# Kernel tuning notes

Hardware: AMD Instinct MI355X
Metric: run time of the kernel (lower is better)

The kernel has to match this reference:

```python
import jax, jax.numpy as jnp
import numpy as np

N_EMBED = 1024
N_HEAD = 16
HEAD_SIZE = N_EMBED // N_HEAD  # 64
SEQ = 2048
BATCH = 2
EPS = 1e-5


def setup_inputs() -> dict:
    key = jax.random.key(0)
    ks = jax.random.split(key, 16)
    s = lambda fan_in: 1.0 / np.sqrt(fan_in)
    d, h, hs, f = N_EMBED, N_HEAD, HEAD_SIZE, 4 * N_EMBED
    return {
        "x": jax.random.normal(ks[0], (BATCH, SEQ, d), dtype=jnp.float32),
        # per-head QKV projections (no bias), stacked over heads: [H, D, hs]
        "wq": jax.random.normal(ks[1], (h, d, hs), dtype=jnp.float32) * s(d),
        "wk": jax.random.normal(ks[2], (h, d, hs), dtype=jnp.float32) * s(d),
        "wv": jax.random.normal(ks[3], (h, d, hs), dtype=jnp.float32) * s(d),
        "w_proj": jax.random.normal(ks[4], (d, d), dtype=jnp.float32) * s(d),
        "b_proj": jnp.zeros((d,), dtype=jnp.float32),
        "w1": jax.random.normal(ks[5], (d, f), dtype=jnp.float32) * s(d),
        "b1": jnp.zeros((f,), dtype=jnp.float32),
        "w2": jax.random.normal(ks[6], (f, d), dtype=jnp.float32) * s(f),
        "b2": jnp.zeros((d,), dtype=jnp.float32),
        "g1": jnp.ones((d,), dtype=jnp.float32),
        "be1": jnp.zeros((d,), dtype=jnp.float32),
        "g2": jnp.ones((d,), dtype=jnp.float32),
        "be2": jnp.zeros((d,), dtype=jnp.float32),
    }


def _layer_norm(x, gamma, beta):
    mu = jnp.mean(x, axis=-1, keepdims=True)
    var = jnp.mean(jnp.square(x - mu), axis=-1, keepdims=True)
    return (x - mu) * jax.lax.rsqrt(var + EPS) * gamma + beta


def reference(x, wq, wk, wv, w_proj, b_proj, w1, b1, w2, b2, g1, be1, g2, be2):
    B, S, D = x.shape
    # per-head projections (vectorized over heads): [B, H, S, hs]
    q = jnp.einsum("bsd,hdk->bhsk", x, wq)
    k = jnp.einsum("bsd,hdk->bhsk", x, wk)
    v = jnp.einsum("bsd,hdk->bhsk", x, wv)
    scale = HEAD_SIZE ** -0.5
    scores = jnp.einsum("bhsk,bhtk->bhst", q, k) * scale  # [B,H,S,S]
    causal = jnp.tril(jnp.ones((S, S), dtype=bool))
    scores = jnp.where(causal, scores, -jnp.inf)
    w = jax.nn.softmax(scores, axis=-1)  # dropout=0 -> identity
    attn = jnp.einsum("bhst,bhtk->bhsk", w, v)  # [B,H,S,hs]
    # concat heads (head-major ordering matches torch.cat over heads)
    attn = attn.transpose(0, 2, 1, 3).reshape(B, S, D)
    y = attn @ w_proj + b_proj
    x = _layer_norm(x + y, g1, be1)
    y = jax.nn.relu(x @ w1 + b1) @ w2 + b2
    x = _layer_norm(x + y, g2, be2)
    return x
```

## Files before the change

kernel.cpp:

```cpp
#include <hip/hip_runtime.h>


typedef unsigned short u16;
typedef unsigned int u32;
typedef __attribute__((ext_vector_type(8))) short bf16x8;
typedef __attribute__((ext_vector_type(4))) float f32x4;
typedef __attribute__((ext_vector_type(2))) u32 u32x2;
typedef __attribute__((ext_vector_type(4))) _Float16 f16x4;

#define MFMA16(a, b, c) __builtin_amdgcn_mfma_f32_16x16x32_bf16(a, b, c, 0, 0, 0)
#define MFMAH(a, b, c) __builtin_amdgcn_mfma_f32_16x16x16f16(a, b, c, 0, 0, 0)

__device__ __forceinline__ u16 f2b(float f) {
  unsigned int u = __builtin_bit_cast(unsigned int, f);
  u = (u + 0x7fffu + ((u >> 16) & 1u)) >> 16;
  return (u16)u;
}

__device__ __forceinline__ void gload_lds16(const u16* g, u16* l) {
  __builtin_amdgcn_global_load_lds((const __attribute__((address_space(1))) void*)g,
                                   (__attribute__((address_space(3))) void*)l, 16, 0, 0);
}

__device__ __forceinline__ u32 pkrtz(float lo, float hi) {
  return __builtin_bit_cast(u32, __builtin_amdgcn_cvt_pkrtz(lo, hi));
}

__device__ __forceinline__ f16x4 pack4h(float a, float b, float c, float d) {
  u32x2 r = {pkrtz(a, b), pkrtz(c, d)};
  return __builtin_bit_cast(f16x4, r);
}


__global__ __launch_bounds__(256) void castx_kernel(const float* __restrict__ src,
                                                    u16* __restrict__ dst) {
  int i = (blockIdx.x * 256 + threadIdx.x) * 4;
  float4 v = *(const float4*)(src + i);
  dst[i + 0] = f2b(v.x);
  dst[i + 1] = f2b(v.y);
  dst[i + 2] = f2b(v.z);
  dst[i + 3] = f2b(v.w);
}

__global__ __launch_bounds__(256) void tcast_kernel(const float* __restrict__ src,
                                                    u16* __restrict__ dst, int R, int C) {
  __shared__ float tile[32][33];
  int tx = threadIdx.x, ty = threadIdx.y;
  int r0 = blockIdx.y * 32, c0 = blockIdx.x * 32;
#pragma unroll
  for (int i = 0; i < 4; ++i)
    tile[ty + i * 8][tx] = src[(size_t)(r0 + ty + i * 8) * C + c0 + tx];
  __syncthreads();
#pragma unroll
  for (int i = 0; i < 4; ++i)
    dst[(size_t)(c0 + ty + i * 8) * R + r0 + tx] = f2b(tile[tx][ty + i * 8]);
}

__global__ __launch_bounds__(256) void tcast_qkv_kernel(const float* __restrict__ wq,
                                                        const float* __restrict__ wk,
                                                        const float* __restrict__ wv,
                                                        u16* __restrict__ dst) {
  __shared__ float tile[32][33];
  int tx = threadIdx.x, ty = threadIdx.y;
  int z = blockIdx.z;
  int p = z >> 4, h = z & 15;
  const float* src = (p == 0 ? wq : (p == 1 ? wk : wv)) + (size_t)h * 1024 * 64;
  float scale = (p == 0) ? 0.1803368801f : 1.0f;
  u16* dbase = dst + (size_t)(p * 1024 + h * 64) * 1024;
  int r0 = blockIdx.y * 32, c0 = blockIdx.x * 32;
#pragma unroll
  for (int i = 0; i < 4; ++i)
    tile[ty + i * 8][tx] = src[(size_t)(r0 + ty + i * 8) * 64 + c0 + tx];
  __syncthreads();
#pragma unroll
  for (int i = 0; i < 4; ++i)
    dbase[(size_t)(c0 + ty + i * 8) * 1024 + r0 + tx] = f2b(tile[tx][ty + i * 8] * scale);
}


template <int MODE, int BN>
__global__ __launch_bounds__(256) void gemm_bf16(const u16* __restrict__ A,
                                                 const u16* __restrict__ Bt, int M, int N,
                                                 int K, const float* __restrict__ bias,
                                                 const float* __restrict__ resid,
                                                 u16* __restrict__ outB,
                                                 float* __restrict__ outF, int ldc,
                                                 u16* __restrict__ vtg) {
  constexpr int BM = 128, BK = 64;
  constexpr int IM = (BN == 128) ? 4 : 2;
  constexpr int JN = 4;
  __shared__ u16 As[BM * BK];
  __shared__ u16 Bs[BN * BK];
  int t = threadIdx.x;
  int m0 = blockIdx.y * BM, n0 = blockIdx.x * BN;
  int lane = t & 63, wid = t >> 6;
  int wm = (BN == 128) ? (wid >> 1) * 64 : wid * 32;
  int wn = (BN == 128) ? (wid & 1) * 64 : 0;
  int m16 = lane & 15, quad = lane >> 4;
  int sw = m16 & 7;

  f32x4 acc[IM][JN] = {};

  for (int k0 = 0; k0 < K; k0 += BK) {
    __syncthreads();
#pragma unroll
    for (int i = 0; i < 4; ++i) {
      int S = i * 256 + t;
      int row = S >> 3, c = S & 7;
      gload_lds16(&A[(size_t)(m0 + row) * K + k0 + (c ^ (row & 7)) * 8],
                  &As[(i * 256 + wid * 64) * 8]);
    }
#pragma unroll
    for (int i = 0; i < BN / 32; ++i) {
      int S = i * 256 + t;
      int row = S >> 3, c = S & 7;
      gload_lds16(&Bt[(size_t)(n0 + row) * K + k0 + (c ^ (row & 7)) * 8],
                  &Bs[(i * 256 + wid * 64) * 8]);
    }
    __syncthreads();
#pragma unroll
    for (int kk = 0; kk < 2; ++kk) {
      bf16x8 af[IM], bfr[JN];
      int slot = (kk * 4 + quad) ^ sw;
#pragma unroll
      for (int i = 0; i < IM; ++i)
        af[i] = *(const bf16x8*)&As[(wm + i * 16 + m16) * BK + slot * 8];
#pragma unroll
      for (int j = 0; j < JN; ++j)
        bfr[j] = *(const bf16x8*)&Bs[(wn + j * 16 + m16) * BK + slot * 8];
#pragma unroll
      for (int i = 0; i < IM; ++i)
#pragma unroll
        for (int j = 0; j < JN; ++j) acc[i][j] = MFMA16(af[i], bfr[j], acc[i][j]);
    }
  }

  if (MODE == 3 && n0 >= 2048) {
#pragma unroll
    for (int i = 0; i < IM; ++i)
#pragma unroll
      for (int j = 0; j < JN; ++j) {
        int dg = n0 + wn + j * 16 + m16 - 2048;
        int hh = dg >> 6, dd = dg & 63;
        int token = m0 + wm + i * 16 + quad * 4;
        int bb = token >> 11, tt = token & 2047;
        u32x2 pv = {pkrtz(acc[i][j][0], acc[i][j][1]),
                    pkrtz(acc[i][j][2], acc[i][j][3])};
        *(u32x2*)&vtg[(((size_t)bb * 16 + hh) * 64 + dd) * 2048 + tt] = pv;
      }
    return;
  }

#pragma unroll
  for (int i = 0; i < IM; ++i)
#pragma unroll
    for (int j = 0; j < JN; ++j) {
      int col = n0 + wn + j * 16 + m16;
      float bv = (MODE == 0 || MODE == 3) ? 0.0f : bias[col];
#pragma unroll
      for (int r = 0; r < 4; ++r) {
        int row = m0 + wm + i * 16 + quad * 4 + r;
        float v = acc[i][j][r];
        if (MODE == 1 || MODE == 2) v += bv;
        if (MODE == 1) v = v > 0.0f ? v : 0.0f;
        if (MODE == 2) {
          v += resid[(size_t)row * ldc + col];
          outF[(size_t)row * ldc + col] = v;
        } else {
          outB[(size_t)row * ldc + col] = f2b(v);
        }
      }
    }
}


__global__ __launch_bounds__(256) void attn_kernel(const u16* __restrict__ qk,
                                                   const u16* __restrict__ vtg,
                                                   u16* __restrict__ attn_out) {
  int bid = blockIdx.x;
  int r = bid < 256 ? bid : 767 - bid;
  int qblock = 15 - (r >> 5);
  int pair = r & 31;
  int h = pair & 15, b = pair >> 4;
  int t = threadIdx.x, lane = t & 63, w = t >> 6;
  int m16 = lane & 15, quad = lane >> 4;
  int qb0 = qblock * 128;
  int wq0 = qb0 + w * 32;

  __shared__ u16 Ks[2][64 * 64];
  __shared__ u16 Vs[2][64 * 64];

  bf16x8 qa[2][2];
#pragma unroll
  for (int qs = 0; qs < 2; ++qs) {
    const u16* qp = qk + (size_t)(b * 2048 + wq0 + qs * 16 + m16) * 2048 + h * 64;
    qa[qs][0] = *(const bf16x8*)&qp[quad * 8];
    qa[qs][1] = *(const bf16x8*)&qp[32 + quad * 8];
  }

  f32x4 oT[2][4] = {};
  f32x4 lacc[2] = {};
  float mrun = -1e30f;

  int iters = 2 * qblock + 2;
  int row0 = t >> 3, c0 = t & 7;
  int row1 = 32 + row0;
  const u16* kbase = qk + (size_t)(b * 2048) * 2048 + 1024 + h * 64;
  const u16* vbase = vtg + ((size_t)(b * 16 + h) * 64) * 2048;
  int sw = m16 & 7;

#define STAGE_ASYNC(IT, BUF)                                                          \
  {                                                                                   \
    int tt0 = (IT) * 64;                                                              \
    gload_lds16(&kbase[(size_t)(tt0 + row0) * 2048 + (c0 ^ (row0 & 7)) * 8],          \
                &Ks[BUF][(w * 64) * 8]);                                              \
    gload_lds16(&kbase[(size_t)(tt0 + row1) * 2048 + (c0 ^ (row1 & 7)) * 8],          \
                &Ks[BUF][(256 + w * 64) * 8]);                                        \
    gload_lds16(&vbase[(size_t)row0 * 2048 + tt0 + (c0 ^ (row0 & 7)) * 8],            \
                &Vs[BUF][(w * 64) * 8]);                                              \
    gload_lds16(&vbase[(size_t)row1 * 2048 + tt0 + (c0 ^ (row1 & 7)) * 8],            \
                &Vs[BUF][(256 + w * 64) * 8]);                                        \
  }

  STAGE_ASYNC(0, 0);
  __syncthreads();

  for (int it = 0; it < iters; ++it) {
    int t0 = it * 64;
    int cur = it & 1;
    if (it + 1 < iters) STAGE_ASYNC(it + 1, !cur);

    if (t0 <= wq0 + 31) {
      f32x4 sv[2][4];
#pragma unroll
      for (int ts = 0; ts < 4; ++ts) {
        bf16x8 ka0 = *(const bf16x8*)&Ks[cur][(ts * 16 + m16) * 64 + (quad ^ sw) * 8];
        bf16x8 ka1 =
            *(const bf16x8*)&Ks[cur][(ts * 16 + m16) * 64 + ((4 + quad) ^ sw) * 8];
#pragma unroll
        for (int qs = 0; qs < 2; ++qs) {
          f32x4 a = {};
          a = MFMA16(ka0, qa[qs][0], a);
          a = MFMA16(ka1, qa[qs][1], a);
          sv[qs][ts] = a;
        }
      }
      if (t0 + 63 > wq0) {
#pragma unroll
        for (int qs = 0; qs < 2; ++qs)
#pragma unroll
          for (int ts = 0; ts < 4; ++ts)
#pragma unroll
            for (int rr = 0; rr < 4; ++rr) {
              int key = t0 + ts * 16 + quad * 4 + rr;
              if (key > wq0 + qs * 16 + m16) sv[qs][ts][rr] = -3e38f;
            }
      }
      f32x4 m4 = sv[0][0];
#pragma unroll
      for (int qs = 0; qs < 2; ++qs)
#pragma unroll
        for (int ts = 0; ts < 4; ++ts) {
          if (qs == 0 && ts == 0) continue;
#pragma unroll
          for (int rr = 0; rr < 4; ++rr) m4[rr] = fmaxf(m4[rr], sv[qs][ts][rr]);
        }
      float mx = fmaxf(fmaxf(m4[0], m4[1]), fmaxf(m4[2], m4[3]));
#pragma unroll
      for (int d = 1; d < 64; d <<= 1) mx = fmaxf(mx, __shfl_xor(mx, d));
      if (mx > mrun) {
        float alpha = exp2f(mrun - mx);
#pragma unroll
        for (int qs = 0; qs < 2; ++qs) {
          lacc[qs] *= alpha;
#pragma unroll
          for (int ds = 0; ds < 4; ++ds) oT[qs][ds] *= alpha;
        }
        mrun = mx;
      }
      f16x4 pf[2][4];
#pragma unroll
      for (int qs = 0; qs < 2; ++qs)
#pragma unroll
        for (int ts = 0; ts < 4; ++ts) {
          float p0 = exp2f(sv[qs][ts][0] - mrun);
          float p1 = exp2f(sv[qs][ts][1] - mrun);
          float p2 = exp2f(sv[qs][ts][2] - mrun);
          float p3 = exp2f(sv[qs][ts][3] - mrun);
          lacc[qs][0] += p0;
          lacc[qs][1] += p1;
          lacc[qs][2] += p2;
          lacc[qs][3] += p3;
          pf[qs][ts] = pack4h(p0, p1, p2, p3);
        }
#pragma unroll
      for (int ts = 0; ts < 4; ++ts)
#pragma unroll
        for (int ds = 0; ds < 4; ++ds) {
          f16x4 av = __builtin_bit_cast(
              f16x4, *(const u32x2*)&Vs[cur][(ds * 16 + m16) * 64 +
                                             (((ts * 2 + (quad >> 1)) ^ sw) * 8) +
                                             (quad & 1) * 4]);
          oT[0][ds] = MFMAH(av, pf[0][ts], oT[0][ds]);
          oT[1][ds] = MFMAH(av, pf[1][ts], oT[1][ds]);
        }
    }
    __syncthreads();
  }
#undef STAGE_ASYNC

#pragma unroll
  for (int qs = 0; qs < 2; ++qs) {
    float ls = lacc[qs][0] + lacc[qs][1] + lacc[qs][2] + lacc[qs][3];
    ls += __shfl_xor(ls, 16);
    ls += __shfl_xor(ls, 32);
    float rl = 1.0f / ls;
    int q = wq0 + qs * 16 + m16;
#pragma unroll
    for (int ds = 0; ds < 4; ++ds) {
      f32x4 o = oT[qs][ds];
      u32x2 ov = {(u32)f2b(o[0] * rl) | ((u32)f2b(o[1] * rl) << 16),
                  (u32)f2b(o[2] * rl) | ((u32)f2b(o[3] * rl) << 16)};
      *(u32x2*)&attn_out[(size_t)(b * 2048 + q) * 1024 + h * 64 + ds * 16 + quad * 4] =
          ov;
    }
  }
}


__global__ __launch_bounds__(256) void ln_kernel(const float* __restrict__ in,
                                                 const float* __restrict__ g,
                                                 const float* __restrict__ be,
                                                 float* __restrict__ outF,
                                                 u16* __restrict__ outB) {
  int row = blockIdx.x;
  int t = threadIdx.x;
  const float* p = in + (size_t)row * 1024 + t * 4;
  float4 v = *(const float4*)p;
  float s = v.x + v.y + v.z + v.w;
  float sq = v.x * v.x + v.y * v.y + v.z * v.z + v.w * v.w;
#pragma unroll
  for (int d = 1; d < 64; d <<= 1) {
    s += __shfl_xor(s, d);
    sq += __shfl_xor(sq, d);
  }
  __shared__ float red[8];
  int lane = t & 63, wid = t >> 6;
  if (lane == 0) {
    red[wid] = s;
    red[4 + wid] = sq;
  }
  __syncthreads();
  s = red[0] + red[1] + red[2] + red[3];
  sq = red[4] + red[5] + red[6] + red[7];
  float mu = s * (1.0f / 1024.0f);
  float var = sq * (1.0f / 1024.0f) - mu * mu;
  float rstd = rsqrtf(var + 1e-5f);
  float4 gv = *(const float4*)(g + t * 4);
  float4 bv = *(const float4*)(be + t * 4);
  float o0 = (v.x - mu) * rstd * gv.x + bv.x;
  float o1 = (v.y - mu) * rstd * gv.y + bv.y;
  float o2 = (v.z - mu) * rstd * gv.z + bv.z;
  float o3 = (v.w - mu) * rstd * gv.w + bv.w;
  size_t o = (size_t)row * 1024 + t * 4;
  if (outF) {
    float4 ov = {o0, o1, o2, o3};
    *(float4*)(outF + o) = ov;
  }
  if (outB) {
    outB[o + 0] = f2b(o0);
    outB[o + 1] = f2b(o1);
    outB[o + 2] = f2b(o2);
    outB[o + 3] = f2b(o3);
  }
}


extern "C" void kernel_launch(void* const* d_in, const int* in_sizes, int n_in,
                              void* d_out, int out_size, void* d_ws, size_t ws_size,
                              hipStream_t stream) {
  const float* x = (const float*)d_in[0];
  const float* wq = (const float*)d_in[1];
  const float* wk = (const float*)d_in[2];
  const float* wv = (const float*)d_in[3];
  const float* w_proj = (const float*)d_in[4];
  const float* b_proj = (const float*)d_in[5];
  const float* w1 = (const float*)d_in[6];
  const float* b1 = (const float*)d_in[7];
  const float* w2 = (const float*)d_in[8];
  const float* b2 = (const float*)d_in[9];
  const float* g1 = (const float*)d_in[10];
  const float* be1 = (const float*)d_in[11];
  const float* g2 = (const float*)d_in[12];
  const float* be2 = (const float*)d_in[13];
  float* out = (float*)d_out;

  const int M = 4096;
  char* w = (char*)d_ws;
  u16* Xbf = (u16*)w;        w += (size_t)M * 1024 * 2;
  u16* WqkvT = (u16*)w;      w += (size_t)3072 * 1024 * 2;
  u16* WprojT = (u16*)w;     w += (size_t)1024 * 1024 * 2;
  u16* W1T = (u16*)w;        w += (size_t)4096 * 1024 * 2;
  u16* W2T = (u16*)w;        w += (size_t)1024 * 4096 * 2;
  u16* QK = (u16*)w;         w += (size_t)M * 2048 * 2;
  u16* Vtg = (u16*)w;        w += (size_t)2 * 16 * 64 * 2048 * 2;
  u16* Attn = (u16*)w;       w += (size_t)M * 1024 * 2;
  float* X1f = (float*)w;    w += (size_t)M * 1024 * 4;
  u16* X1b = (u16*)w;        w += (size_t)M * 1024 * 2;
  u16* Hbuf = QK;

  castx_kernel<<<M * 1024 / 1024, 256, 0, stream>>>(x, Xbf);
  tcast_qkv_kernel<<<dim3(2, 32, 48), dim3(32, 8), 0, stream>>>(wq, wk, wv, WqkvT);
  tcast_kernel<<<dim3(32, 32), dim3(32, 8), 0, stream>>>(w_proj, WprojT, 1024, 1024);
  tcast_kernel<<<dim3(128, 32), dim3(32, 8), 0, stream>>>(w1, W1T, 1024, 4096);
  tcast_kernel<<<dim3(32, 128), dim3(32, 8), 0, stream>>>(w2, W2T, 4096, 1024);

  gemm_bf16<3, 128><<<dim3(3072 / 128, M / 128), 256, 0, stream>>>(
      Xbf, WqkvT, M, 3072, 1024, nullptr, nullptr, QK, nullptr, 2048, Vtg);

  attn_kernel<<<512, 256, 0, stream>>>(QK, Vtg, Attn);

  gemm_bf16<2, 64><<<dim3(1024 / 64, M / 128), 256, 0, stream>>>(
      Attn, WprojT, M, 1024, 1024, b_proj, x, nullptr, out, 1024, nullptr);

  ln_kernel<<<M, 256, 0, stream>>>(out, g1, be1, X1f, X1b);

  gemm_bf16<1, 128><<<dim3(4096 / 128, M / 128), 256, 0, stream>>>(
      X1b, W1T, M, 4096, 1024, b1, nullptr, Hbuf, nullptr, 4096, nullptr);

  gemm_bf16<2, 64><<<dim3(1024 / 64, M / 128), 256, 0, stream>>>(
      Hbuf, W2T, M, 1024, 4096, b2, X1f, nullptr, out, 1024, nullptr);

  ln_kernel<<<M, 256, 0, stream>>>(out, g2, be2, out, nullptr);
}
```

Measured before the change: 357.5 us.

## Split causal attention across key segments with flash-decoding style combine

Replaces the single attention kernel with a split-K version: each 128-query block is divided into up to four 512-key segments, giving 1280 work items scheduled in a longest-first order from constant tables. Partial outputs (fp16) and per-row max/sum are written to scratch reusing the X1f buffer, and a second kernel merges the segments with rescaling. Per-row running max replaces the per-warp max. This aims to fix load imbalance and low occupancy from causal masking, at the cost of an extra launch, scratch traffic and fp16 rounding of unnormalized partials.

```diff
diff --git a/kernel.cpp b/kernel.cpp
--- a/kernel.cpp
+++ b/kernel.cpp
@@ -174,18 +174,38 @@
 }
 
 
-__global__ __launch_bounds__(256) void attn_kernel(const u16* __restrict__ qk,
-                                                   const u16* __restrict__ vtg,
-                                                   u16* __restrict__ attn_out) {
-  int bid = blockIdx.x;
-  int r = bid < 256 ? bid : 767 - bid;
-  int qblock = 15 - (r >> 5);
-  int pair = r & 31;
-  int h = pair & 15, b = pair >> 4;
+__constant__ unsigned char SLOT_LPT[40] = {
+    3, 4, 6, 8, 10, 11, 12, 13, 15, 16, 18, 19, 21, 22, 23, 24, 25, 26, 28, 29,
+    30, 32, 33, 34, 36, 37, 38, 39,
+    2, 9, 20, 35,
+    1, 7, 17, 31,
+    0, 5, 14, 27};
+__constant__ unsigned char SLOT_QB[40] = {0, 1, 2, 3, 4, 4, 5, 5, 6, 6, 7, 7, 8, 8,
+                                          8, 9, 9, 9, 10, 10, 10, 11, 11, 11, 12, 12,
+                                          12, 12, 13, 13, 13, 13, 14, 14, 14, 14, 15,
+                                          15, 15, 15};
+__constant__ unsigned char SLOT_S[40] = {0, 0, 0, 0, 0, 1, 0, 1, 0, 1, 0, 1, 0, 1,
+                                         2, 0, 1, 2, 0, 1, 2, 0, 1, 2, 0, 1, 2, 3,
+                                         0, 1, 2, 3, 0, 1, 2, 3, 0, 1, 2, 3};
+__constant__ unsigned char QB_BASE[16] = {0, 1, 2, 3, 4, 6, 8, 10,
+                                          12, 15, 18, 21, 24, 28, 32, 36};
+
+__global__ __launch_bounds__(256) void attn_part(const u16* __restrict__ qk,
+                                                 const u16* __restrict__ vtg,
+                                                 u16* __restrict__ opart,
+                                                 float2* __restrict__ ml) {
+  int rank = blockIdx.x >> 5, bh = blockIdx.x & 31;
+  int slot = SLOT_LPT[rank];
+  int qb = SLOT_QB[slot], s = SLOT_S[slot];
+  int b = bh >> 4, h = bh & 15;
+  int nseg = (qb >> 2) + 1;
+  int k_start = s * 512;
+  int k_end = min((s + 1) * 512, (qb + 1) * 128);
+  int iters = (k_end - k_start) >> 6;
+
   int t = threadIdx.x, lane = t & 63, w = t >> 6;
   int m16 = lane & 15, quad = lane >> 4;
-  int qb0 = qblock * 128;
-  int wq0 = qb0 + w * 32;
+  int wq0 = qb * 128 + w * 32;
 
   __shared__ u16 Ks[2][64 * 64];
   __shared__ u16 Vs[2][64 * 64];
@@ -200,35 +220,33 @@
 
   f32x4 oT[2][4] = {};
   f32x4 lacc[2] = {};
-  float mrun = -1e30f;
-
-  int iters = 2 * qblock + 2;
+  float mrun[2] = {-1e30f, -1e30f};
+
   int row0 = t >> 3, c0 = t & 7;
   int row1 = 32 + row0;
   const u16* kbase = qk + (size_t)(b * 2048) * 2048 + 1024 + h * 64;
   const u16* vbase = vtg + ((size_t)(b * 16 + h) * 64) * 2048;
   int sw = m16 & 7;
 
-#define STAGE_ASYNC(IT, BUF)                                                          \
-  {                                                                                   \
-    int tt0 = (IT) * 64;                                                              \
-    gload_lds16(&kbase[(size_t)(tt0 + row0) * 2048 + (c0 ^ (row0 & 7)) * 8],          \
-                &Ks[BUF][(w * 64) * 8]);                                              \
-    gload_lds16(&kbase[(size_t)(tt0 + row1) * 2048 + (c0 ^ (row1 & 7)) * 8],          \
-                &Ks[BUF][(256 + w * 64) * 8]);                                        \
-    gload_lds16(&vbase[(size_t)row0 * 2048 + tt0 + (c0 ^ (row0 & 7)) * 8],            \
-                &Vs[BUF][(w * 64) * 8]);                                              \
-    gload_lds16(&vbase[(size_t)row1 * 2048 + tt0 + (c0 ^ (row1 & 7)) * 8],            \
-                &Vs[BUF][(256 + w * 64) * 8]);                                        \
-  }
-
-  STAGE_ASYNC(0, 0);
+#define STAGE_ASYNC(T0, BUF)                                                        \
+  {                                                                                 \
+    gload_lds16(&kbase[(size_t)((T0) + row0) * 2048 + (c0 ^ (row0 & 7)) * 8],       \
+                &Ks[BUF][(w * 64) * 8]);                                            \
+    gload_lds16(&kbase[(size_t)((T0) + row1) * 2048 + (c0 ^ (row1 & 7)) * 8],       \
+                &Ks[BUF][(256 + w * 64) * 8]);                                      \
+    gload_lds16(&vbase[(size_t)row0 * 2048 + (T0) + (c0 ^ (row0 & 7)) * 8],         \
+                &Vs[BUF][(w * 64) * 8]);                                            \
+    gload_lds16(&vbase[(size_t)row1 * 2048 + (T0) + (c0 ^ (row1 & 7)) * 8],         \
+                &Vs[BUF][(256 + w * 64) * 8]);                                      \
+  }
+
+  STAGE_ASYNC(k_start, 0);
   __syncthreads();
 
   for (int it = 0; it < iters; ++it) {
-    int t0 = it * 64;
+    int t0 = k_start + it * 64;
     int cur = it & 1;
-    if (it + 1 < iters) STAGE_ASYNC(it + 1, !cur);
+    if (it + 1 < iters) STAGE_ASYNC(t0 + 64, !cur);
 
     if (t0 <= wq0 + 31) {
       f32x4 sv[2][4];
@@ -256,37 +274,32 @@
               if (key > wq0 + qs * 16 + m16) sv[qs][ts][rr] = -3e38f;
             }
       }
-      f32x4 m4 = sv[0][0];
-#pragma unroll
-      for (int qs = 0; qs < 2; ++qs)
-#pragma unroll
-        for (int ts = 0; ts < 4; ++ts) {
-          if (qs == 0 && ts == 0) continue;
-#pragma unroll
-          for (int rr = 0; rr < 4; ++rr) m4[rr] = fmaxf(m4[rr], sv[qs][ts][rr]);
-        }
-      float mx = fmaxf(fmaxf(m4[0], m4[1]), fmaxf(m4[2], m4[3]));
-#pragma unroll
-      for (int d = 1; d < 64; d <<= 1) mx = fmaxf(mx, __shfl_xor(mx, d));
-      if (mx > mrun) {
-        float alpha = exp2f(mrun - mx);
-#pragma unroll
-        for (int qs = 0; qs < 2; ++qs) {
-          lacc[qs] *= alpha;
-#pragma unroll
-          for (int ds = 0; ds < 4; ++ds) oT[qs][ds] *= alpha;
-        }
-        mrun = mx;
+#pragma unroll
+      for (int qs = 0; qs < 2; ++qs) {
+        float mx = fmaxf(fmaxf(sv[qs][0][0], sv[qs][0][1]),
+                         fmaxf(sv[qs][0][2], sv[qs][0][3]));
+#pragma unroll
+        for (int ts = 1; ts < 4; ++ts)
+          mx = fmaxf(mx, fmaxf(fmaxf(sv[qs][ts][0], sv[qs][ts][1]),
+                               fmaxf(sv[qs][ts][2], sv[qs][ts][3])));
+        mx = fmaxf(mx, __shfl_xor(mx, 16));
+        mx = fmaxf(mx, __shfl_xor(mx, 32));
+        float mnew = fmaxf(mrun[qs], mx);
+        float alpha = exp2f(mrun[qs] - mnew);
+        mrun[qs] = mnew;
+        lacc[qs] *= alpha;
+#pragma unroll
+        for (int ds = 0; ds < 4; ++ds) oT[qs][ds] *= alpha;
       }
       f16x4 pf[2][4];
 #pragma unroll
       for (int qs = 0; qs < 2; ++qs)
 #pragma unroll
         for (int ts = 0; ts < 4; ++ts) {
-          float p0 = exp2f(sv[qs][ts][0] - mrun);
-          float p1 = exp2f(sv[qs][ts][1] - mrun);
-          float p2 = exp2f(sv[qs][ts][2] - mrun);
-          float p3 = exp2f(sv[qs][ts][3] - mrun);
+          float p0 = exp2f(sv[qs][ts][0] - mrun[qs]);
+          float p1 = exp2f(sv[qs][ts][1] - mrun[qs]);
+          float p2 = exp2f(sv[qs][ts][2] - mrun[qs]);
+          float p3 = exp2f(sv[qs][ts][3] - mrun[qs]);
           lacc[qs][0] += p0;
           lacc[qs][1] += p1;
           lacc[qs][2] += p2;
@@ -309,21 +322,64 @@
   }
 #undef STAGE_ASYNC
 
+  size_t sbase = ((size_t)bh * 40 + slot) * 128;
 #pragma unroll
   for (int qs = 0; qs < 2; ++qs) {
     float ls = lacc[qs][0] + lacc[qs][1] + lacc[qs][2] + lacc[qs][3];
     ls += __shfl_xor(ls, 16);
     ls += __shfl_xor(ls, 32);
-    float rl = 1.0f / ls;
-    int q = wq0 + qs * 16 + m16;
+    int qloc = w * 32 + qs * 16 + m16;
 #pragma unroll
     for (int ds = 0; ds < 4; ++ds) {
       f32x4 o = oT[qs][ds];
-      u32x2 ov = {(u32)f2b(o[0] * rl) | ((u32)f2b(o[1] * rl) << 16),
-                  (u32)f2b(o[2] * rl) | ((u32)f2b(o[3] * rl) << 16)};
-      *(u32x2*)&attn_out[(size_t)(b * 2048 + q) * 1024 + h * 64 + ds * 16 + quad * 4] =
-          ov;
-    }
+      u32x2 ov = {pkrtz(o[0], o[1]), pkrtz(o[2], o[3])};
+      *(u32x2*)&opart[(sbase + qloc) * 64 + ds * 16 + quad * 4] = ov;
+    }
+    if (quad == 0) ml[sbase + qloc] = make_float2(mrun[qs], ls);
+  }
+}
+
+__global__ __launch_bounds__(256) void attn_comb(const u16* __restrict__ opart,
+                                                 const float2* __restrict__ ml,
+                                                 u16* __restrict__ attn_out) {
+  int qb = blockIdx.x, bh = blockIdx.y;
+  int b = bh >> 4, h = bh & 15;
+  int nseg = (qb >> 2) + 1;
+  int base = QB_BASE[qb];
+  int t = threadIdx.x;
+  int q = t >> 1, dh = (t & 1) * 32;
+
+  float m[4], l[4], wgt[4];
+  float M = -3e38f;
+  for (int s = 0; s < nseg; ++s) {
+    float2 v = ml[((size_t)bh * 40 + base + s) * 128 + q];
+    m[s] = v.x;
+    l[s] = v.y;
+    M = fmaxf(M, v.x);
+  }
+  float lsum = 0.0f;
+  for (int s = 0; s < nseg; ++s) {
+    wgt[s] = exp2f(m[s] - M);
+    lsum += wgt[s] * l[s];
+  }
+  float rl = 1.0f / lsum;
+
+  size_t orow = (size_t)(b * 2048 + qb * 128 + q) * 1024 + h * 64 + dh;
+#pragma unroll 2
+  for (int dd = 0; dd < 32; dd += 4) {
+    float o0 = 0, o1 = 0, o2 = 0, o3 = 0;
+    for (int s = 0; s < nseg; ++s) {
+      f16x4 hv = __builtin_bit_cast(
+          f16x4,
+          *(const u32x2*)&opart[(((size_t)bh * 40 + base + s) * 128 + q) * 64 + dh + dd]);
+      o0 += wgt[s] * (float)hv[0];
+      o1 += wgt[s] * (float)hv[1];
+      o2 += wgt[s] * (float)hv[2];
+      o3 += wgt[s] * (float)hv[3];
+    }
+    u32x2 ov = {(u32)f2b(o0 * rl) | ((u32)f2b(o1 * rl) << 16),
+                (u32)f2b(o2 * rl) | ((u32)f2b(o3 * rl) << 16)};
+    *(u32x2*)&attn_out[orow + dd] = ov;
   }
 }
 
@@ -408,6 +464,8 @@
   float* X1f = (float*)w;    w += (size_t)M * 1024 * 4;
   u16* X1b = (u16*)w;        w += (size_t)M * 1024 * 2;
   u16* Hbuf = QK;
+  u16* Opart = (u16*)X1f;
+  float2* Ml = (float2*)((char*)X1f + (size_t)1280 * 8192 * 2);
 
   castx_kernel<<<M * 1024 / 1024, 256, 0, stream>>>(x, Xbf);
   tcast_qkv_kernel<<<dim3(2, 32, 48), dim3(32, 8), 0, stream>>>(wq, wk, wv, WqkvT);
@@ -418,7 +476,8 @@
   gemm_bf16<3, 128><<<dim3(3072 / 128, M / 128), 256, 0, stream>>>(
       Xbf, WqkvT, M, 3072, 1024, nullptr, nullptr, QK, nullptr, 2048, Vtg);
 
-  attn_kernel<<<512, 256, 0, stream>>>(QK, Vtg, Attn);
+  attn_part<<<1280, 256, 0, stream>>>(QK, Vtg, Opart, Ml);
+  attn_comb<<<dim3(16, 32), 256, 0, stream>>>(Opart, Ml, Attn);
 
   gemm_bf16<2, 64><<<dim3(1024 / 64, M / 128), 256, 0, stream>>>(
       Attn, WprojT, M, 1024, 1024, b_proj, x, nullptr, out, 1024, nullptr);
```

New measurement: 370.3 us. 1.04x slower.
